# Performance work log

Hardware: AMD Instinct MI355X
Metric: run time of the kernel (lower is better)

The kernel has to match this reference:

```python
import jax, jax.numpy as jnp
import numpy as np

FEATURE_DIM = 63
DIM = 64
B, N = 1024, 256


def setup_inputs() -> dict:
    key = jax.random.key(0)
    ks = jax.random.split(key, 10)
    # padded batched dense adjacency [B, N, N] (includes self-loops + supernode edges in real data)
    adj = (jax.random.uniform(ks[0], (B, N, N), dtype=jnp.float32) < 0.05).astype(jnp.float32)
    adj = adj + jnp.eye(N, dtype=jnp.float32)[None]  # self loops as in process()
    vec = jax.random.normal(ks[1], (B, N, FEATURE_DIM), dtype=jnp.float32)
    s1 = 1.0 / np.sqrt(FEATURE_DIM)
    s2 = 1.0 / np.sqrt(DIM)
    return {
        "adj": adj,
        "vec": vec,
        "w1_rel": jax.random.normal(ks[2], (FEATURE_DIM, DIM), dtype=jnp.float32) * s1,
        "w1_root": jax.random.normal(ks[3], (FEATURE_DIM, DIM), dtype=jnp.float32) * s1,
        "b1": jnp.zeros((DIM,), dtype=jnp.float32),
        "w2_rel": jax.random.normal(ks[4], (DIM, DIM), dtype=jnp.float32) * s2,
        "w2_root": jax.random.normal(ks[5], (DIM, DIM), dtype=jnp.float32) * s2,
        "b2": jnp.zeros((DIM,), dtype=jnp.float32),
        "wf": jax.random.normal(ks[6], (DIM, 2), dtype=jnp.float32) * s2,
        "bf": jnp.zeros((2,), dtype=jnp.float32),
    }


def dense_graph_conv(adj, x, w_rel, w_root, b):
    # PyG DenseGraphConv: lin_rel(adj @ x) + lin_root(x)
    agg = jnp.einsum('bij,bjf->bif', adj, x)  # [B,N,F] neighbor aggregation
    return agg @ w_rel + x @ w_root + b


def reference(adj, vec, w1_rel, w1_root, b1, w2_rel, w2_root, b2, wf, bf):
    x = jax.nn.relu(dense_graph_conv(adj, vec, w1_rel, w1_root, b1))  # [B,N,dim]
    y = jax.nn.relu(dense_graph_conv(adj, x, w2_rel, w2_root, b2))    # [B,N,dim]
    # readout at node 0 (virtual supernode), then linear head -> [B,2]
    return (x[:, 0] + y[:, 0]) @ wf + bf
```

## Files before the change

kernel.cpp:

```cpp
#include <hip/hip_runtime.h>


#define NB 1024
#define NN 256
#define FD 63
#define DM 64
#define MAXP 32
#define VT 264
#define W72 72

using short8 = __attribute__((ext_vector_type(8))) short;
using f32x4  = __attribute__((ext_vector_type(4))) float;

__device__ __forceinline__ short f2bf(float f) {
    unsigned u = __builtin_bit_cast(unsigned, f);
    return (short)((u + 0x7FFFu + ((u >> 16) & 1u)) >> 16);
}

__global__ void k0_w1frag(const float* __restrict__ w1_rel,
                          const float* __restrict__ w1_root,
                          short8* __restrict__ outR,
                          short8* __restrict__ outO)
{
    const int fi = blockIdx.x * blockDim.x + threadIdx.x;
    if (fi >= 512) return;
    const int lane = fi & 63, ksn = fi >> 6;
    const int ks = ksn & 1, nt = ksn >> 1;
    const int n  = (lane & 15) + 16 * nt;
    const int kb = ks * 32 + (lane >> 4) * 8;
    short8 r, o;
    #pragma unroll
    for (int u = 0; u < 8; ++u) {
        const int k = kb + u;
        const bool ok = (k < FD);
        r[u] = ok ? f2bf(w1_rel[k * DM + n])  : (short)0;
        o[u] = ok ? f2bf(w1_root[k * DM + n]) : (short)0;
    }
    outR[fi] = r;
    outO[fi] = o;
}

__launch_bounds__(256, 3)
__global__ void gnn_node0_mfma(const float* __restrict__ adj,
                               const float* __restrict__ vec,
                               const float* __restrict__ b1,
                               const float* __restrict__ w2_rel,
                               const float* __restrict__ w2_root,
                               const float* __restrict__ b2,
                               const float* __restrict__ wf,
                               const float* __restrict__ bf,
                               const short8* __restrict__ w1fR,
                               const short8* __restrict__ w1fO,
                               float* __restrict__ out)
{
    __shared__ __align__(16) short s_vecT[DM * VT];
    __shared__ __align__(16) short s_aggb[MAXP * W72];
    __shared__ float s_accp[4][DM];
    __shared__ float s_pA[4][DM];
    __shared__ float s_rA[DM], s_rB[DM], s_r[DM];
    __shared__ float s_a0[MAXP];
    __shared__ int   s_nbr[MAXP];
    __shared__ int   s_cnt, s_p0;

    const int b    = blockIdx.x;
    const int t    = threadIdx.x;
    const int lane = t & 63;
    const int q    = t >> 6;
    const int lr   = lane & 15;
    const int lg   = lane >> 4;
    const int mt   = q & 1;
    const int ntb  = (q >> 1) * 2;
    const float* adj_b = adj + (size_t)b * NN * NN;
    const float* vec_b = vec + (size_t)b * NN * FD;

    if (t == 0) { s_cnt = 0; s_p0 = 0; }
    if (t < MAXP) { s_a0[t] = 0.f; s_nbr[t] = 0; }
    __syncthreads();

    {
        float a = adj_b[t];
        if (a != 0.f) {
            int idx = atomicAdd(&s_cnt, 1);
            if (idx < MAXP) { s_nbr[idx] = t; s_a0[idx] = a; if (t == 0) s_p0 = idx; }
        }
    }
    __syncthreads();

    const int jmine = s_nbr[lr + 16 * mt];
    f32x4 araw[16];
    {
        const float* rp = adj_b + (size_t)jmine * NN + lg * 8;
        #pragma unroll
        for (int ks = 0; ks < 8; ++ks) {
            araw[2 * ks]     = *reinterpret_cast<const f32x4*>(rp + ks * 32);
            araw[2 * ks + 1] = *reinterpret_cast<const f32x4*>(rp + ks * 32 + 4);
        }
    }

    if (lane < FD) {
        const int kb0 = q * 64;
        #pragma unroll 2
        for (int r0 = 0; r0 < 64; r0 += 8) {
            float v[8];
            #pragma unroll
            for (int u = 0; u < 8; ++u) v[u] = vec_b[(kb0 + r0 + u) * FD + lane];
            short8 sv;
            #pragma unroll
            for (int u = 0; u < 8; ++u) sv[u] = f2bf(v[u]);
            *reinterpret_cast<short8*>(&s_vecT[lane * VT + kb0 + r0]) = sv;
        }
    }
    for (int i = t; i < NN; i += 256) s_vecT[63 * VT + i] = 0;

    short8 afrag[8];
    #pragma unroll
    for (int ks = 0; ks < 8; ++ks) {
        short8 s;
        #pragma unroll
        for (int u = 0; u < 4; ++u) {
            s[u]     = f2bf(araw[2 * ks][u]);
            s[4 + u] = f2bf(araw[2 * ks + 1][u]);
        }
        afrag[ks] = s;
    }
    __syncthreads();

    const int p0 = s_p0;

    {
        f32x4 acc0 = {0.f, 0.f, 0.f, 0.f};
        f32x4 acc1 = {0.f, 0.f, 0.f, 0.f};
        const short* b0p = &s_vecT[(lr + 16 * ntb) * VT + lg * 8];
        const short* b1p = &s_vecT[(lr + 16 * ntb + 16) * VT + lg * 8];
        #pragma unroll
        for (int ks = 0; ks < 8; ++ks) {
            const short8 bf0 = *reinterpret_cast<const short8*>(b0p + ks * 32);
            const short8 bf1 = *reinterpret_cast<const short8*>(b1p + ks * 32);
            acc0 = __builtin_amdgcn_mfma_f32_16x16x32_bf16(afrag[ks], bf0, acc0, 0, 0, 0);
            acc1 = __builtin_amdgcn_mfma_f32_16x16x32_bf16(afrag[ks], bf1, acc1, 0, 0, 0);
        }
        #pragma unroll
        for (int r = 0; r < 4; ++r) {
            const int row = lg * 4 + r + 16 * mt;
            s_aggb[row * W72 + lr + 16 * ntb]      = f2bf(acc0[r]);
            s_aggb[row * W72 + lr + 16 * ntb + 16] = f2bf(acc1[r]);
        }
    }
    __syncthreads();

    {
        f32x4 acc0 = {0.f, 0.f, 0.f, 0.f};
        f32x4 acc1 = {0.f, 0.f, 0.f, 0.f};
        const int prow = lr + 16 * mt;
        const int jsel = s_nbr[prow];
        const short* aggrow = &s_aggb[prow * W72 + lg * 8];
        #pragma unroll
        for (int ks = 0; ks < 2; ++ks) {
            const int ko = ks * 32 + lg * 8;
            const short8 aA = *reinterpret_cast<const short8*>(aggrow + ks * 32);
            short8 aV;
            #pragma unroll
            for (int u = 0; u < 8; ++u)
                aV[u] = s_vecT[(ko + u) * VT + jsel];
            const short8 vR0 = w1fR[((ntb    ) * 2 + ks) * 64 + lane];
            const short8 vR1 = w1fR[((ntb + 1) * 2 + ks) * 64 + lane];
            const short8 vO0 = w1fO[((ntb    ) * 2 + ks) * 64 + lane];
            const short8 vO1 = w1fO[((ntb + 1) * 2 + ks) * 64 + lane];
            acc0 = __builtin_amdgcn_mfma_f32_16x16x32_bf16(aA, vR0, acc0, 0, 0, 0);
            acc0 = __builtin_amdgcn_mfma_f32_16x16x32_bf16(aV, vO0, acc0, 0, 0, 0);
            acc1 = __builtin_amdgcn_mfma_f32_16x16x32_bf16(aA, vR1, acc1, 0, 0, 0);
            acc1 = __builtin_amdgcn_mfma_f32_16x16x32_bf16(aV, vO1, acc1, 0, 0, 0);
        }
        const int c0 = lr + 16 * ntb, c1 = c0 + 16;
        const float bc0 = b1[c0], bc1 = b1[c1];
        float aY0 = 0.f, aY1 = 0.f;
        #pragma unroll
        for (int r = 0; r < 4; ++r) {
            const int row = lg * 4 + r + 16 * mt;
            const float a0 = s_a0[row];
            const float x0v = fmaxf(acc0[r] + bc0, 0.f);
            const float x1v = fmaxf(acc1[r] + bc1, 0.f);
            aY0 += a0 * x0v;
            aY1 += a0 * x1v;
            if (row == p0) { s_rB[c0] = x0v; s_rB[c1] = x1v; }
        }
        aY0 += __shfl_xor(aY0, 16); aY0 += __shfl_xor(aY0, 32);
        aY1 += __shfl_xor(aY1, 16); aY1 += __shfl_xor(aY1, 32);
        if (lg == 0) { s_accp[q][c0] = aY0; s_accp[q][c1] = aY1; }
    }
    __syncthreads();

    if (q == 0) {
        const int qp = 2 * (lane >> 5);
        s_rA[lane] = s_accp[qp][lane] + s_accp[qp + 1][lane];
    }
    __syncthreads();

    {
        float p = 0.f;
        const int f0 = q * 16;
        #pragma unroll
        for (int ff2 = 0; ff2 < 16; ++ff2) {
            const int ff = f0 + ff2;
            p += s_rA[ff] * w2_rel[ff * DM + lane]
               + s_rB[ff] * w2_root[ff * DM + lane];
        }
        s_pA[q][lane] = p;
    }
    __syncthreads();
    if (t < DM) {
        const float y = fmaxf(s_pA[0][t] + s_pA[1][t] + s_pA[2][t] + s_pA[3][t] + b2[t], 0.f);
        s_r[t] = s_rB[t] + y;
    }
    __syncthreads();
    if (t < 2) {
        float acc = bf[t];
        #pragma unroll
        for (int d = 0; d < DM; ++d) acc += s_r[d] * wf[d * 2 + t];
        out[b * 2 + t] = acc;
    }
}

extern "C" void kernel_launch(void* const* d_in, const int* in_sizes, int n_in,
                              void* d_out, int out_size, void* d_ws, size_t ws_size,
                              hipStream_t stream) {
    const float* adj     = (const float*)d_in[0];
    const float* vec     = (const float*)d_in[1];
    const float* w1_rel  = (const float*)d_in[2];
    const float* w1_root = (const float*)d_in[3];
    const float* b1      = (const float*)d_in[4];
    const float* w2_rel  = (const float*)d_in[5];
    const float* w2_root = (const float*)d_in[6];
    const float* b2      = (const float*)d_in[7];
    const float* wf      = (const float*)d_in[8];
    const float* bf      = (const float*)d_in[9];
    float* out = (float*)d_out;

    short8* wsR = (short8*)d_ws;
    short8* wsO = wsR + 512;

    k0_w1frag<<<2, 256, 0, stream>>>(w1_rel, w1_root, wsR, wsO);
    gnn_node0_mfma<<<NB, 256, 0, stream>>>(adj, vec, b1, w2_rel, w2_root,
                                           b2, wf, bf, wsR, wsO, out);
}
```

Before: 357.5 us.

## Coalesce vec loads as float4 and restrict adj-row fetch to two waves

The vec tile is now read as contiguous float4 chunks across all threads and scattered into the transposed bf16 LDS layout with div-by-63 index math, replacing strided per-feature scalar loads. The first aggregation GEMM is remapped so only two waves each load one 16-row adjacency slab and compute all four column tiles. Before, every wave loaded an adjacency slab, so each slab was fetched twice. This removes the duplicate adjacency reads and improves global coalescing. In exchange it adds scattered 2-byte LDS stores with possible bank conflicts, and leaves half the waves idle during the first MFMA stage.

```diff
diff --git a/kernel.cpp b/kernel.cpp
--- a/kernel.cpp
+++ b/kernel.cpp
@@ -8,6 +8,7 @@
 #define MAXP 32
 #define VT 264
 #define W72 72
+#define NF4 4032
 
 using short8 = __attribute__((ext_vector_type(8))) short;
 using f32x4  = __attribute__((ext_vector_type(4))) float;
@@ -68,8 +69,6 @@
     const int q    = t >> 6;
     const int lr   = lane & 15;
     const int lg   = lane >> 4;
-    const int mt   = q & 1;
-    const int ntb  = (q >> 1) * 2;
     const float* adj_b = adj + (size_t)b * NN * NN;
     const float* vec_b = vec + (size_t)b * NN * FD;
 
@@ -86,10 +85,10 @@
     }
     __syncthreads();
 
-    const int jmine = s_nbr[lr + 16 * mt];
     f32x4 araw[16];
-    {
-        const float* rp = adj_b + (size_t)jmine * NN + lg * 8;
+    if (q < 2) {
+        const int jm = s_nbr[lr + 16 * q];
+        const float* rp = adj_b + (size_t)jm * NN + lg * 8;
         #pragma unroll
         for (int ks = 0; ks < 8; ++ks) {
             araw[2 * ks]     = *reinterpret_cast<const f32x4*>(rp + ks * 32);
@@ -97,60 +96,88 @@
         }
     }
 
-    if (lane < FD) {
-        const int kb0 = q * 64;
-        #pragma unroll 2
-        for (int r0 = 0; r0 < 64; r0 += 8) {
-            float v[8];
+    {
+        const f32x4* vf4 = reinterpret_cast<const f32x4*>(vec_b);
+        #pragma unroll
+        for (int g = 0; g < 4; ++g) {
+            const int base = t + g * 1024;
+            f32x4 v0 = {0,0,0,0}, v1 = {0,0,0,0}, v2 = {0,0,0,0}, v3 = {0,0,0,0};
+            const bool o0 = base            < NF4;
+            const bool o1 = base + 256      < NF4;
+            const bool o2 = base + 512      < NF4;
+            const bool o3 = base + 768      < NF4;
+            if (o0) v0 = vf4[base];
+            if (o1) v1 = vf4[base + 256];
+            if (o2) v2 = vf4[base + 512];
+            if (o3) v3 = vf4[base + 768];
             #pragma unroll
-            for (int u = 0; u < 8; ++u) v[u] = vec_b[(kb0 + r0 + u) * FD + lane];
-            short8 sv;
+            for (int u = 0; u < 4; ++u) {
+                const int ii = base + u * 256;
+                if (ii >= NF4) break;
+                const f32x4 v = (u == 0) ? v0 : (u == 1) ? v1 : (u == 2) ? v2 : v3;
+                const int ee = ii * 4;
+                int k = ee / 63;
+                int f = ee - k * 63;
+                #pragma unroll
+                for (int w = 0; w < 4; ++w) {
+                    s_vecT[f * VT + k] = f2bf(v[w]);
+                    if (++f == FD) { f = 0; ++k; }
+                }
+            }
+        }
+        for (int i = t; i < NN; i += 256) s_vecT[63 * VT + i] = 0;
+    }
+
+    short8 afrag[8];
+    if (q < 2) {
+        #pragma unroll
+        for (int ks = 0; ks < 8; ++ks) {
+            short8 s;
             #pragma unroll
-            for (int u = 0; u < 8; ++u) sv[u] = f2bf(v[u]);
-            *reinterpret_cast<short8*>(&s_vecT[lane * VT + kb0 + r0]) = sv;
-        }
-    }
-    for (int i = t; i < NN; i += 256) s_vecT[63 * VT + i] = 0;
-
-    short8 afrag[8];
-    #pragma unroll
-    for (int ks = 0; ks < 8; ++ks) {
-        short8 s;
-        #pragma unroll
-        for (int u = 0; u < 4; ++u) {
-            s[u]     = f2bf(araw[2 * ks][u]);
-            s[4 + u] = f2bf(araw[2 * ks + 1][u]);
-        }
-        afrag[ks] = s;
+            for (int u = 0; u < 4; ++u) {
+                s[u]     = f2bf(araw[2 * ks][u]);
+                s[4 + u] = f2bf(araw[2 * ks + 1][u]);
+            }
+            afrag[ks] = s;
+        }
     }
     __syncthreads();
 
     const int p0 = s_p0;
 
-    {
-        f32x4 acc0 = {0.f, 0.f, 0.f, 0.f};
-        f32x4 acc1 = {0.f, 0.f, 0.f, 0.f};
-        const short* b0p = &s_vecT[(lr + 16 * ntb) * VT + lg * 8];
-        const short* b1p = &s_vecT[(lr + 16 * ntb + 16) * VT + lg * 8];
+    if (q < 2) {
+        f32x4 A0 = {0,0,0,0}, A1 = {0,0,0,0}, A2 = {0,0,0,0}, A3 = {0,0,0,0};
+        const short* b0p = &s_vecT[(lr     ) * VT + lg * 8];
+        const short* b1p = &s_vecT[(lr + 16) * VT + lg * 8];
+        const short* b2p = &s_vecT[(lr + 32) * VT + lg * 8];
+        const short* b3p = &s_vecT[(lr + 48) * VT + lg * 8];
         #pragma unroll
         for (int ks = 0; ks < 8; ++ks) {
-            const short8 bf0 = *reinterpret_cast<const short8*>(b0p + ks * 32);
-            const short8 bf1 = *reinterpret_cast<const short8*>(b1p + ks * 32);
-            acc0 = __builtin_amdgcn_mfma_f32_16x16x32_bf16(afrag[ks], bf0, acc0, 0, 0, 0);
-            acc1 = __builtin_amdgcn_mfma_f32_16x16x32_bf16(afrag[ks], bf1, acc1, 0, 0, 0);
+            const short8 f0 = *reinterpret_cast<const short8*>(b0p + ks * 32);
+            const short8 f1 = *reinterpret_cast<const short8*>(b1p + ks * 32);
+            const short8 f2 = *reinterpret_cast<const short8*>(b2p + ks * 32);
+            const short8 f3 = *reinterpret_cast<const short8*>(b3p + ks * 32);
+            A0 = __builtin_amdgcn_mfma_f32_16x16x32_bf16(afrag[ks], f0, A0, 0, 0, 0);
+            A1 = __builtin_amdgcn_mfma_f32_16x16x32_bf16(afrag[ks], f1, A1, 0, 0, 0);
+            A2 = __builtin_amdgcn_mfma_f32_16x16x32_bf16(afrag[ks], f2, A2, 0, 0, 0);
+            A3 = __builtin_amdgcn_mfma_f32_16x16x32_bf16(afrag[ks], f3, A3, 0, 0, 0);
         }
         #pragma unroll
         for (int r = 0; r < 4; ++r) {
-            const int row = lg * 4 + r + 16 * mt;
-            s_aggb[row * W72 + lr + 16 * ntb]      = f2bf(acc0[r]);
-            s_aggb[row * W72 + lr + 16 * ntb + 16] = f2bf(acc1[r]);
-        }
-    }
-    __syncthreads();
-
-    {
-        f32x4 acc0 = {0.f, 0.f, 0.f, 0.f};
-        f32x4 acc1 = {0.f, 0.f, 0.f, 0.f};
+            const int row = lg * 4 + r + 16 * q;
+            s_aggb[row * W72 + lr     ] = f2bf(A0[r]);
+            s_aggb[row * W72 + lr + 16] = f2bf(A1[r]);
+            s_aggb[row * W72 + lr + 32] = f2bf(A2[r]);
+            s_aggb[row * W72 + lr + 48] = f2bf(A3[r]);
+        }
+    }
+    __syncthreads();
+
+    {
+        const int mt  = q & 1;
+        const int ntb = (q >> 1) * 2;
+        f32x4 acc0 = {0,0,0,0};
+        f32x4 acc1 = {0,0,0,0};
         const int prow = lr + 16 * mt;
         const int jsel = s_nbr[prow];
         const short* aggrow = &s_aggb[prow * W72 + lg * 8];
```

Measured after the change: 359.3 us. Within noise of the previous version (+0.5%).
